# Kernel tuning notes

Measured on AMD Instinct MI355X. Metric: run time of the kernel, lower is better.

The kernel has to match this reference:

```python
import jax, jax.numpy as jnp
import numpy as np

D_MODEL = 1024
N_HEADS = 16
N_KV = 8
GROUP = N_HEADS // N_KV  # 2
D_HEAD = D_MODEL // N_HEADS  # 64
SCALE = D_HEAD ** -0.5


def setup_inputs() -> dict:
    key = jax.random.key(0)
    ks = jax.random.split(key, 5)
    s = 0.02
    return {
        "x": jax.random.normal(ks[0], (2, 2048, D_MODEL), dtype=jnp.float32),
        "Wq": jax.random.normal(ks[1], (D_MODEL, D_MODEL), dtype=jnp.float32) * s,
        "Wk": jax.random.normal(ks[2], (N_KV * D_HEAD, D_MODEL), dtype=jnp.float32) * s,
        "Wv": jax.random.normal(ks[3], (N_KV * D_HEAD, D_MODEL), dtype=jnp.float32) * s,
        "Wproj": jax.random.normal(ks[4], (D_MODEL, D_MODEL), dtype=jnp.float32) * s,
    }


def reference(x, Wq, Wk, Wv, Wproj):
    b, t, c = x.shape
    # projections (torch Linear: x @ W.T)
    q = (x @ Wq.T).reshape(b, t, N_KV, GROUP, D_HEAD)  # heads ordered (kv, group)
    k = (x @ Wk.T).reshape(b, t, N_KV, D_HEAD)
    v = (x @ Wv.T).reshape(b, t, N_KV, D_HEAD)
    # repeat_interleave(K/V, group, dim=heads) == broadcast over the group axis,
    # since q head index h maps to kv head h // GROUP.
    scores = jnp.einsum('btkgd,bskd->bkgts', q, k) * SCALE  # (b, kv, g, t, s)
    attn = jax.nn.softmax(scores, axis=-1)
    y = jnp.einsum('bkgts,bskd->btkgd', attn, v)  # (b, t, kv, g, d)
    y = y.reshape(b, t, c)
    return y @ Wproj.T
```

## Files before the change

### kernel.cpp

```cpp
#include <hip/hip_runtime.h>


#define SEQ    2048
#define CDIM   1024
#define KVDIM  512
#define SCL2E  0.18033688011112042f

typedef __attribute__((ext_vector_type(8))) short   bf16x8;
typedef __attribute__((ext_vector_type(4))) float   f32x4;
typedef unsigned short ushort_t;

__device__ __forceinline__ ushort_t f2bf(float f) {
    unsigned u = __float_as_uint(f);
    u += 0x7FFFu + ((u >> 16) & 1u);
    return (ushort_t)(u >> 16);
}
__device__ __forceinline__ float bf2f(ushort_t h) {
    return __uint_as_float(((unsigned)h) << 16);
}
__device__ __forceinline__ void load_lds16(const void* g, void* l) {
    __builtin_amdgcn_global_load_lds(
        (const __attribute__((address_space(1))) void*)g,
        (__attribute__((address_space(3))) void*)l, 16, 0, 0);
}

__global__ __launch_bounds__(256) void cvt_bf16(
    const float* __restrict__ x,  const float* __restrict__ wq,
    const float* __restrict__ wk, const float* __restrict__ wv,
    const float* __restrict__ wp,
    ushort_t* __restrict__ xh,  ushort_t* __restrict__ wqh,
    ushort_t* __restrict__ wkh, ushort_t* __restrict__ wvh,
    ushort_t* __restrict__ wph)
{
    const int i = blockIdx.x * 256 + threadIdx.x;
    const float* src; ushort_t* dst; int off;
    if (i < 1048576)      { src = x;  dst = xh;  off = i; }
    else if (i < 1310720) { src = wq; dst = wqh; off = i - 1048576; }
    else if (i < 1441792) { src = wk; dst = wkh; off = i - 1310720; }
    else if (i < 1572864) { src = wv; dst = wvh; off = i - 1441792; }
    else                  { src = wp; dst = wph; off = i - 1572864; }
    const float4 v = ((const float4*)src)[off];
    ushort4 h;
    h.x = f2bf(v.x); h.y = f2bf(v.y); h.z = f2bf(v.z); h.w = f2bf(v.w);
    ((ushort4*)dst)[off] = h;
}

__global__ __launch_bounds__(256, 4) void gemm64(
    const ushort_t* __restrict__ A, int K,
    const ushort_t* __restrict__ B1, void* __restrict__ C1, int N1, int epi1, float sc1,
    const ushort_t* __restrict__ B2, void* __restrict__ C2, int N2, int epi2, float sc2,
    const ushort_t* __restrict__ B3, void* __restrict__ C3, int N3, int epi3, float sc3)
{
    __shared__ ushort_t sA[128 * 64];
    __shared__ ushort_t sB[64 * 64];

    const int tid = threadIdx.x, wv = tid >> 6, lane = tid & 63;
    const int lm = lane & 15, quad = lane >> 4;

    const int gdx = gridDim.x;
    const int nwg = gdx * gridDim.y;
    int id = blockIdx.y * gdx + blockIdx.x;
    id = (id & 7) * (nwg >> 3) + (id >> 3);
    const int bx = id % gdx;
    const int m0 = (id / gdx) * 128;

    const int t1 = N1 >> 6, t2 = N2 >> 6;
    const ushort_t* B; void* Cv; int n0, Nout, epi; float sc;
    if (bx < t1)           { B = B1; Cv = C1; Nout = N1; epi = epi1; sc = sc1; n0 = bx * 64; }
    else if (bx < t1 + t2) { B = B2; Cv = C2; Nout = N2; epi = epi2; sc = sc2; n0 = (bx - t1) * 64; }
    else                   { B = B3; Cv = C3; Nout = N3; epi = epi3; sc = sc3; n0 = (bx - t1 - t2) * 64; }

    const int mh = wv >> 1, nh = wv & 1;
    const int srow = lane >> 3;
    const int scol = ((lane & 7) ^ ((lane >> 3) & 7)) * 8;

    f32x4 acc[4][2] = {};

    for (int k0 = 0; k0 < K; k0 += 64) {
        __syncthreads();
        #pragma unroll
        for (int i = 0; i < 6; ++i) {
            const int g = wv * 6 + i;
            if (g < 16)
                load_lds16(A + (size_t)(m0 + g * 8 + srow) * K + k0 + scol, sA + g * 512);
            else
                load_lds16(B + (size_t)(n0 + (g - 16) * 8 + srow) * K + k0 + scol, sB + (g - 16) * 512);
        }
        __syncthreads();

        #pragma unroll
        for (int ks = 0; ks < 2; ++ks) {
            const int co = ((ks * 4 + quad) ^ (lm & 7)) * 8;
            bf16x8 a[4], b[2];
            #pragma unroll
            for (int mt = 0; mt < 4; ++mt)
                a[mt] = *(const bf16x8*)&sA[(mh * 64 + mt * 16 + lm) * 64 + co];
            #pragma unroll
            for (int nt = 0; nt < 2; ++nt)
                b[nt] = *(const bf16x8*)&sB[(nh * 32 + nt * 16 + lm) * 64 + co];
            #pragma unroll
            for (int mt = 0; mt < 4; ++mt)
                #pragma unroll
                for (int nt = 0; nt < 2; ++nt)
                    acc[mt][nt] = __builtin_amdgcn_mfma_f32_16x16x32_bf16(a[mt], b[nt], acc[mt][nt], 0, 0, 0);
        }
    }

    if (epi == 0) {
        float* C = (float*)Cv;
        #pragma unroll
        for (int mt = 0; mt < 4; ++mt)
            #pragma unroll
            for (int nt = 0; nt < 2; ++nt)
                #pragma unroll
                for (int r = 0; r < 4; ++r)
                    C[(size_t)(m0 + mh * 64 + mt * 16 + quad * 4 + r) * Nout + n0 + nh * 32 + nt * 16 + lm]
                        = acc[mt][nt][r];
    } else if (epi == 2) {
        ushort_t* C = (ushort_t*)Cv;
        const int bB   = m0 >> 11;
        const int tloc = (m0 & 2047) + mh * 64 + quad * 4;
        #pragma unroll
        for (int mt = 0; mt < 4; ++mt)
            #pragma unroll
            for (int nt = 0; nt < 2; ++nt) {
                const int n = n0 + nh * 32 + nt * 16 + lm;
                ushort4 u;
                u.x = f2bf(acc[mt][nt][0]);
                u.y = f2bf(acc[mt][nt][1]);
                u.z = f2bf(acc[mt][nt][2]);
                u.w = f2bf(acc[mt][nt][3]);
                *(ushort4*)&C[(size_t)(bB * KVDIM + n) * SEQ + tloc + mt * 16] = u;
            }
    } else {
        ushort_t* C = (ushort_t*)Cv;
        #pragma unroll
        for (int mt = 0; mt < 4; ++mt)
            #pragma unroll
            for (int nt = 0; nt < 2; ++nt)
                #pragma unroll
                for (int r = 0; r < 4; ++r)
                    C[(size_t)(m0 + mh * 64 + mt * 16 + quad * 4 + r) * Nout + n0 + nh * 32 + nt * 16 + lm]
                        = f2bf(acc[mt][nt][r] * sc);
    }
}

__global__ __launch_bounds__(256, 4) void attn6(
    const ushort_t* __restrict__ Qh, const ushort_t* __restrict__ Kh,
    const ushort_t* __restrict__ Vth, ushort_t* __restrict__ Yh)
{
    __shared__ ushort_t sK[2][64 * 64];
    __shared__ ushort_t sV[2][64 * 64];

    const int tid = threadIdx.x, wv = tid >> 6, lane = tid & 63;
    const int lm = lane & 15, quad = lane >> 4;
    const int b = blockIdx.y >> 4, h = blockIdx.y & 15, kvh = h >> 1;
    const int t0 = blockIdx.x * 64, tq0 = t0 + wv * 16;

    bf16x8 qh[2];
    {
        const size_t rb = (size_t)(b * SEQ + tq0 + lm) * CDIM + h * 64;
        #pragma unroll
        for (int ks = 0; ks < 2; ++ks)
            qh[ks] = *(const bf16x8*)(Qh + rb + ks * 32 + quad * 8);
    }

    const ushort_t* gK = Kh  + (size_t)b * SEQ * KVDIM + kvh * 64;
    const ushort_t* gV = Vth + (size_t)(b * 8 + kvh) * 64 * SEQ;

    const int g0 = (wv & 1) * 4;
    const int srow = lane >> 3;
    const int scol = ((lane & 7) ^ ((lane >> 3) & 7)) * 8;

    int krow[4];
    #pragma unroll
    for (int it = 0; it < 4; ++it) {
        const int lr = (g0 + it) * 8 + srow;
        krow[it] = (lr & 0x20) | ((lr & 0x10) >> 2) | ((lr & 0x0C) << 1) | (lr & 3);
    }

    float l_r = 0.0f;
    f32x4 O[4] = {};

    if (wv < 2) {
        #pragma unroll
        for (int it = 0; it < 4; ++it)
            load_lds16(gK + (size_t)krow[it] * KVDIM + scol, &sK[0][(g0 + it) * 512]);
    } else {
        #pragma unroll
        for (int it = 0; it < 4; ++it)
            load_lds16(gV + (size_t)((g0 + it) * 8 + srow) * SEQ + scol, &sV[0][(g0 + it) * 512]);
    }

    typedef union { bf16x8 v; unsigned u[4]; } pku;

    for (int kt = 0; kt < SEQ / 64; ++kt) {
        const int cur = kt & 1;
        __syncthreads();

        if (kt + 1 < SEQ / 64) {
            const int s1 = (kt + 1) * 64;
            if (wv < 2) {
                #pragma unroll
                for (int it = 0; it < 4; ++it)
                    load_lds16(gK + (size_t)(s1 + krow[it]) * KVDIM + scol,
                               &sK[cur ^ 1][(g0 + it) * 512]);
            } else {
                #pragma unroll
                for (int it = 0; it < 4; ++it)
                    load_lds16(gV + (size_t)((g0 + it) * 8 + srow) * SEQ + s1 + scol,
                               &sV[cur ^ 1][(g0 + it) * 512]);
            }
        }

        f32x4 st[4] = {};
        __builtin_amdgcn_s_setprio(1);
        #pragma unroll
        for (int sti = 0; sti < 4; ++sti)
            #pragma unroll
            for (int ks = 0; ks < 2; ++ks) {
                const int off = (sti * 16 + lm) * 64 + (((ks * 4 + quad) ^ (lm & 7)) * 8);
                const bf16x8 kf = *(const bf16x8*)&sK[cur][off];
                st[sti] = __builtin_amdgcn_mfma_f32_16x16x32_bf16(kf, qh[ks], st[sti], 0, 0, 0);
            }
        __builtin_amdgcn_s_setprio(0);

        pku pa[2];
        #pragma unroll
        for (int sti = 0; sti < 4; ++sti) {
            const float p0 = __builtin_amdgcn_exp2f(st[sti][0]);
            const float p1 = __builtin_amdgcn_exp2f(st[sti][1]);
            const float p2 = __builtin_amdgcn_exp2f(st[sti][2]);
            const float p3 = __builtin_amdgcn_exp2f(st[sti][3]);
            l_r += (p0 + p1) + (p2 + p3);
            pa[sti >> 1].u[(sti & 1) * 2 + 0] =
                __builtin_amdgcn_perm(__float_as_uint(p1), __float_as_uint(p0), 0x07060302u);
            pa[sti >> 1].u[(sti & 1) * 2 + 1] =
                __builtin_amdgcn_perm(__float_as_uint(p3), __float_as_uint(p2), 0x07060302u);
        }

        __builtin_amdgcn_s_setprio(1);
        #pragma unroll
        for (int ks = 0; ks < 2; ++ks) {
            const int co = ((ks * 4 + quad) ^ (lm & 7)) * 8;
            #pragma unroll
            for (int dt = 0; dt < 4; ++dt) {
                const bf16x8 vt = *(const bf16x8*)&sV[cur][(dt * 16 + lm) * 64 + co];
                O[dt] = __builtin_amdgcn_mfma_f32_16x16x32_bf16(pa[ks].v, vt, O[dt], 0, 0, 0);
            }
        }
        __builtin_amdgcn_s_setprio(0);
    }

    l_r += __shfl_xor(l_r, 16);
    l_r += __shfl_xor(l_r, 32);
    #pragma unroll
    for (int r = 0; r < 4; ++r) {
        const float lq = __shfl(l_r, (lane & 48) | (quad * 4 + r));
        const float inv = 1.0f / lq;
        const int t = tq0 + quad * 4 + r;
        const size_t rowb = (size_t)(b * SEQ + t) * CDIM + h * 64;
        #pragma unroll
        for (int dt = 0; dt < 4; ++dt)
            Yh[rowb + dt * 16 + lm] = f2bf(O[dt][r] * inv);
    }
}

extern "C" void kernel_launch(void* const* d_in, const int* in_sizes, int n_in,
                              void* d_out, int out_size, void* d_ws, size_t ws_size,
                              hipStream_t stream)
{
    const float* x     = (const float*)d_in[0];
    const float* Wq    = (const float*)d_in[1];
    const float* Wk    = (const float*)d_in[2];
    const float* Wv    = (const float*)d_in[3];
    const float* Wproj = (const float*)d_in[4];
    float* out = (float*)d_out;

    const int M = 2 * SEQ;

    char* p = (char*)d_ws;
    ushort_t* xh   = (ushort_t*)p; p += (size_t)M * CDIM * 2;
    ushort_t* wqh  = (ushort_t*)p; p += (size_t)CDIM * CDIM * 2;
    ushort_t* wkh  = (ushort_t*)p; p += (size_t)KVDIM * CDIM * 2;
    ushort_t* wvh  = (ushort_t*)p; p += (size_t)KVDIM * CDIM * 2;
    ushort_t* wph  = (ushort_t*)p; p += (size_t)CDIM * CDIM * 2;
    ushort_t* qh   = (ushort_t*)p; p += (size_t)M * CDIM * 2;
    ushort_t* kh   = (ushort_t*)p; p += (size_t)M * KVDIM * 2;
    ushort_t* vth  = (ushort_t*)p; p += (size_t)M * KVDIM * 2;
    ushort_t* yh = xh;

    dim3 blk(256);

    cvt_bf16<<<dim3(7168), blk, 0, stream>>>(
        x, Wq, Wk, Wv, Wproj, xh, wqh, wkh, wvh, wph);

    gemm64<<<dim3(32, 32), blk, 0, stream>>>(
        xh, CDIM,
        wqh, qh,  CDIM,  3, SCL2E,
        wkh, kh,  KVDIM, 3, 1.0f,
        wvh, vth, KVDIM, 2, 1.0f);

    attn6<<<dim3(SEQ / 64, 32), blk, 0, stream>>>(qh, kh, vth, yh);

    gemm64<<<dim3(16, 32), blk, 0, stream>>>(
        yh, CDIM,
        wph, out, CDIM, 0, 1.0f,
        nullptr, nullptr, 0, 0, 1.0f,
        nullptr, nullptr, 0, 0, 1.0f);
}
```

Measured before the change: 169.9 us.

## Fuse Q projection into attention kernel, computing Q tile in LDS

The Q projection moves out of the QKV GEMM launch and into the attention kernel. Each block computes its 64x64 Q tile from x and Wq with a double-buffered LDS MFMA loop, then scales it, converts it to bf16 and reloads it as fragments. This removes the global write and read of Q and shrinks the first GEMM grid. The cost is that each attention block does a 1024-deep GEMM before attention starts. The x tile is also recomputed by 16 head blocks instead of being read once, which adds redundant L2 traffic.

After: 170.9 us. Within noise of the previous version (+0.6%).

```diff
diff --git a/kernel.cpp b/kernel.cpp
--- a/kernel.cpp
+++ b/kernel.cpp
@@ -14,9 +14,6 @@
     unsigned u = __float_as_uint(f);
     u += 0x7FFFu + ((u >> 16) & 1u);
     return (ushort_t)(u >> 16);
-}
-__device__ __forceinline__ float bf2f(ushort_t h) {
-    return __uint_as_float(((unsigned)h) << 16);
 }
 __device__ __forceinline__ void load_lds16(const void* g, void* l) {
     __builtin_amdgcn_global_load_lds(
@@ -145,9 +142,10 @@
     }
 }
 
-__global__ __launch_bounds__(256, 4) void attn6(
-    const ushort_t* __restrict__ Qh, const ushort_t* __restrict__ Kh,
-    const ushort_t* __restrict__ Vth, ushort_t* __restrict__ Yh)
+__global__ __launch_bounds__(256, 4) void attn7(
+    const ushort_t* __restrict__ xh, const ushort_t* __restrict__ wqh,
+    const ushort_t* __restrict__ Kh, const ushort_t* __restrict__ Vth,
+    ushort_t* __restrict__ Yh)
 {
     __shared__ ushort_t sK[2][64 * 64];
     __shared__ ushort_t sV[2][64 * 64];
@@ -157,20 +155,76 @@
     const int b = blockIdx.y >> 4, h = blockIdx.y & 15, kvh = h >> 1;
     const int t0 = blockIdx.x * 64, tq0 = t0 + wv * 16;
 
+    const int g0   = (wv & 1) * 4;
+    const int srow = lane >> 3;
+    const int scol = ((lane & 7) ^ ((lane >> 3) & 7)) * 8;
+
+    const ushort_t* gX = xh  + (size_t)(b * SEQ + t0) * CDIM;
+    const ushort_t* gW = wqh + (size_t)(h * 64) * CDIM;
+
+    if (wv < 2) {
+        #pragma unroll
+        for (int it = 0; it < 4; ++it)
+            load_lds16(gX + (size_t)((g0 + it) * 8 + srow) * CDIM + scol,
+                       &sK[0][(g0 + it) * 512]);
+    } else {
+        #pragma unroll
+        for (int it = 0; it < 4; ++it)
+            load_lds16(gW + (size_t)((g0 + it) * 8 + srow) * CDIM + scol,
+                       &sV[0][(g0 + it) * 512]);
+    }
+
+    f32x4 accQ[4] = {};
+    for (int kc = 0; kc < CDIM / 64; ++kc) {
+        const int cur = kc & 1;
+        __syncthreads();
+
+        if (kc + 1 < CDIM / 64) {
+            const int c1 = (kc + 1) * 64;
+            if (wv < 2) {
+                #pragma unroll
+                for (int it = 0; it < 4; ++it)
+                    load_lds16(gX + (size_t)((g0 + it) * 8 + srow) * CDIM + c1 + scol,
+                               &sK[cur ^ 1][(g0 + it) * 512]);
+            } else {
+                #pragma unroll
+                for (int it = 0; it < 4; ++it)
+                    load_lds16(gW + (size_t)((g0 + it) * 8 + srow) * CDIM + c1 + scol,
+                               &sV[cur ^ 1][(g0 + it) * 512]);
+            }
+        }
+
+        #pragma unroll
+        for (int ks = 0; ks < 2; ++ks) {
+            const int co = ((ks * 4 + quad) ^ (lm & 7)) * 8;
+            const bf16x8 a = *(const bf16x8*)&sK[cur][(wv * 16 + lm) * 64 + co];
+            #pragma unroll
+            for (int ng = 0; ng < 4; ++ng) {
+                const bf16x8 bq = *(const bf16x8*)&sV[cur][(ng * 16 + lm) * 64 + co];
+                accQ[ng] = __builtin_amdgcn_mfma_f32_16x16x32_bf16(a, bq, accQ[ng], 0, 0, 0);
+            }
+        }
+    }
+
+    #pragma unroll
+    for (int ng = 0; ng < 4; ++ng)
+        #pragma unroll
+        for (int r = 0; r < 4; ++r) {
+            const int t = wv * 16 + quad * 4 + r;
+            const int d = ng * 16 + lm;
+            sK[0][t * 64 + (((d >> 3) ^ (t & 7)) * 8) + (d & 7)]
+                = f2bf(accQ[ng][r] * SCL2E);
+        }
+    __syncthreads();
+
     bf16x8 qh[2];
-    {
-        const size_t rb = (size_t)(b * SEQ + tq0 + lm) * CDIM + h * 64;
-        #pragma unroll
-        for (int ks = 0; ks < 2; ++ks)
-            qh[ks] = *(const bf16x8*)(Qh + rb + ks * 32 + quad * 8);
-    }
+    #pragma unroll
+    for (int ks = 0; ks < 2; ++ks)
+        qh[ks] = *(const bf16x8*)&sK[0][(wv * 16 + lm) * 64 + (((ks * 4 + quad) ^ (lm & 7)) * 8)];
+    __syncthreads();
 
     const ushort_t* gK = Kh  + (size_t)b * SEQ * KVDIM + kvh * 64;
     const ushort_t* gV = Vth + (size_t)(b * 8 + kvh) * 64 * SEQ;
-
-    const int g0 = (wv & 1) * 4;
-    const int srow = lane >> 3;
-    const int scol = ((lane & 7) ^ ((lane >> 3) & 7)) * 8;
 
     int krow[4];
     #pragma unroll
@@ -285,23 +339,22 @@
     ushort_t* wkh  = (ushort_t*)p; p += (size_t)KVDIM * CDIM * 2;
     ushort_t* wvh  = (ushort_t*)p; p += (size_t)KVDIM * CDIM * 2;
     ushort_t* wph  = (ushort_t*)p; p += (size_t)CDIM * CDIM * 2;
-    ushort_t* qh   = (ushort_t*)p; p += (size_t)M * CDIM * 2;
+    ushort_t* yh   = (ushort_t*)p; p += (size_t)M * CDIM * 2;
     ushort_t* kh   = (ushort_t*)p; p += (size_t)M * KVDIM * 2;
     ushort_t* vth  = (ushort_t*)p; p += (size_t)M * KVDIM * 2;
-    ushort_t* yh = xh;
 
     dim3 blk(256);
 
     cvt_bf16<<<dim3(7168), blk, 0, stream>>>(
         x, Wq, Wk, Wv, Wproj, xh, wqh, wkh, wvh, wph);
 
-    gemm64<<<dim3(32, 32), blk, 0, stream>>>(
+    gemm64<<<dim3(16, 32), blk, 0, stream>>>(
         xh, CDIM,
-        wqh, qh,  CDIM,  3, SCL2E,
         wkh, kh,  KVDIM, 3, 1.0f,
-        wvh, vth, KVDIM, 2, 1.0f);
-
-    attn6<<<dim3(SEQ / 64, 32), blk, 0, stream>>>(qh, kh, vth, yh);
+        wvh, vth, KVDIM, 2, 1.0f,
+        nullptr, nullptr, 0, 0, 1.0f);
+
+    attn7<<<dim3(SEQ / 64, 32), blk, 0, stream>>>(xh, wqh, kh, vth, yh);
 
     gemm64<<<dim3(16, 32), blk, 0, stream>>>(
         yh, CDIM,
```
